# Performance work log

Hardware: AMD Instinct MI355X
Metric: run time of the kernel (lower is better)

Reference implementation:

```python
import jax, jax.numpy as jnp
import numpy as np

B, S, DIM, H = 2, 2048, 1024, 16
HD = DIM // H  # head dim = 64


def setup_inputs() -> dict:
    key = jax.random.key(0)
    ks = jax.random.split(key, 10)
    scale = 1.0 / np.sqrt(DIM)
    x = jax.random.normal(ks[0], (B, S, DIM), dtype=jnp.float32)
    # per-head projection weights stacked over heads: [H, DIM, HD]
    Wq = jax.random.normal(ks[1], (H, DIM, HD), dtype=jnp.float32) * scale
    bq = jax.random.normal(ks[2], (H, HD), dtype=jnp.float32) * 0.01
    Wk = jax.random.normal(ks[3], (H, DIM, HD), dtype=jnp.float32) * scale
    bk = jax.random.normal(ks[4], (H, HD), dtype=jnp.float32) * 0.01
    Wv = jax.random.normal(ks[5], (H, DIM, HD), dtype=jnp.float32) * scale
    bv = jax.random.normal(ks[6], (H, HD), dtype=jnp.float32) * 0.01
    # output linear: [DIM, DIM]
    Wo = jax.random.normal(ks[7], (DIM, DIM), dtype=jnp.float32) * scale
    bo = jax.random.normal(ks[8], (DIM,), dtype=jnp.float32) * 0.01
    return {"x": x, "Wq": Wq, "bq": bq, "Wk": Wk, "bk": bk,
            "Wv": Wv, "bv": bv, "Wo": Wo, "bo": bo}


def reference(x, Wq, bq, Wk, bk, Wv, bv, Wo, bo):
    # per-head projections: [B, H, S, HD]
    q = jnp.einsum('bsd,hde->bhse', x, Wq) + bq[None, :, None, :]
    k = jnp.einsum('bsd,hde->bhse', x, Wk) + bk[None, :, None, :]
    v = jnp.einsum('bsd,hde->bhse', x, Wv) + bv[None, :, None, :]
    # causal attention scores: [B, H, S, S], scaled by sqrt(head_dim)
    scores = jnp.einsum('bhse,bhte->bhst', q, k) / jnp.sqrt(jnp.float32(HD))
    causal = jnp.tril(jnp.ones((S, S), dtype=bool))
    scores = jnp.where(causal[None, None], scores, -jnp.inf)
    attn = jax.nn.softmax(scores, axis=-1)
    out = jnp.einsum('bhst,bhte->bhse', attn, v)  # [B, H, S, HD]
    # concat heads in order -> [B, S, DIM]
    out = out.transpose(0, 2, 1, 3).reshape(B, S, DIM)
    return out @ Wo + bo
```

## Files before the change

### kernel.cpp

```cpp
#include <hip/hip_runtime.h>

typedef _Float16 half8 __attribute__((ext_vector_type(8)));
typedef _Float16 half4 __attribute__((ext_vector_type(4)));
typedef float f32x4 __attribute__((ext_vector_type(4)));

#define MFMA32(a, b, c) __builtin_amdgcn_mfma_f32_16x16x32_f16((a), (b), (c), 0, 0, 0)
#define MFMA16(a, b, c) __builtin_amdgcn_mfma_f32_16x16x16f16((a), (b), (c), 0, 0, 0)

static constexpr int Bc = 2, Sc = 2048, DIMc = 1024, Hc = 16, HDc = 64;
static constexpr int Mc = Bc * Sc;
static constexpr int NQKV = 3 * DIMc;

__device__ __forceinline__ void gl_lds16(const _Float16* g, _Float16* l) {
  __builtin_amdgcn_global_load_lds(
      (const __attribute__((address_space(1))) void*)g,
      (__attribute__((address_space(3))) void*)l, 16, 0, 0);
}


__global__ __launch_bounds__(256) void k_prep_all(
    const float* __restrict__ x, const float* __restrict__ Wq,
    const float* __restrict__ Wk, const float* __restrict__ Wv,
    const float* __restrict__ Wo, _Float16* __restrict__ xh,
    _Float16* __restrict__ WallT, _Float16* __restrict__ WoT) {
  __shared__ float Ls[64 * 65];
  const int bx = blockIdx.x, tid = threadIdx.x;
  if (bx < 2048) {
    const int i = bx * 256 + tid;
    const float4* xf = (const float4*)x;
    float4 a = xf[i * 2], b = xf[i * 2 + 1];
    half8 hv;
    hv[0] = (_Float16)a.x; hv[1] = (_Float16)a.y;
    hv[2] = (_Float16)a.z; hv[3] = (_Float16)a.w;
    hv[4] = (_Float16)b.x; hv[5] = (_Float16)b.y;
    hv[6] = (_Float16)b.z; hv[7] = (_Float16)b.w;
    *(half8*)&xh[(size_t)i * 8] = hv;
    return;
  }
  int b2 = bx - 2048;
  if (b2 < 768) {
    const int dt = b2 & 15, ph = b2 >> 4;
    const int p = ph >> 4, h = ph & 15;
    const float* W = (p == 0) ? Wq : (p == 1) ? Wk : Wv;
    for (int c = tid; c < 4096; c += 256) {
      int dr = c >> 6, e = c & 63;
      Ls[e * 65 + dr] = W[h * 65536 + (dt * 64 + dr) * 64 + e];
    }
    __syncthreads();
    for (int c = tid; c < 4096; c += 256) {
      int e = c >> 6, dr = c & 63;
      WallT[(size_t)(p * 1024 + h * 64 + e) * 1024 + dt * 64 + dr] = (_Float16)Ls[e * 65 + dr];
    }
  } else {
    int b3 = b2 - 768;
    const int dt = b3 & 15, nt = b3 >> 4;
    for (int c = tid; c < 4096; c += 256) {
      int dr = c >> 6, nl = c & 63;
      Ls[nl * 65 + dr] = Wo[(dt * 64 + dr) * 1024 + nt * 64 + nl];
    }
    __syncthreads();
    for (int c = tid; c < 4096; c += 256) {
      int nl = c >> 6, dr = c & 63;
      WoT[(size_t)(nt * 64 + nl) * 1024 + dt * 64 + dr] = (_Float16)Ls[nl * 65 + dr];
    }
  }
}


#define STAGE_AB(buf, kk0)                                                     \
    for (int it = 0; it < 2; ++it) {                                           \
      int idx = it * 256 + tid;                                                \
      int row = idx >> 2, scb = (idx & 3) ^ ((row >> 1) & 3);                  \
      gl_lds16(&A[(size_t)(m0 + row) * DIMc + (kk0) + scb * 8],                \
               &As[buf][(it * 256 + wave * 64) * 8]);                          \
    }                                                                          \
    for (int it = 0; it < 2; ++it) {                                           \
      int idx = it * 256 + tid;                                                \
      int row = idx >> 2, scb = (idx & 3) ^ ((row >> 1) & 3);                  \
      gl_lds16(&Bt[(size_t)(n0 + row) * DIMc + (kk0) + scb * 8],               \
               &Bs[buf][(it * 256 + wave * 64) * 8]);                          \
    }

#define GEMM_CORE_COOP()                                                       \
  __shared__ _Float16 As[2][128 * 32];                                         \
  __shared__ _Float16 Bs[2][128 * 32];                                         \
  const int tid = threadIdx.x;                                                 \
  const int lane = tid & 63, wave = tid >> 6;                                  \
  const int quad = lane >> 4, mr = lane & 15;                                  \
  const int sl = quad ^ ((mr >> 1) & 3);                                       \
  const int wm = wave >> 1, wn = wave & 1;                                     \
  f32x4 acc[4][4];                                                             \
  for (int i = 0; i < 4; i++)                                                  \
    for (int j = 0; j < 4; j++) acc[i][j] = f32x4{0.f, 0.f, 0.f, 0.f};         \
  STAGE_AB(0, 0)                                                               \
  for (int k0 = 0; k0 < DIMc; k0 += 32) {                                      \
    const int cur = (k0 >> 5) & 1;                                             \
    if (k0 + 32 < DIMc) {                                                      \
      STAGE_AB(cur ^ 1, k0 + 32)                                               \
      asm volatile("s_waitcnt vmcnt(4)" ::: "memory");                         \
    } else {                                                                   \
      asm volatile("s_waitcnt vmcnt(0)" ::: "memory");                         \
    }                                                                          \
    __builtin_amdgcn_s_barrier();                                              \
    __builtin_amdgcn_sched_barrier(0);                                         \
    half8 af[4], bf[4];                                                        \
    for (int i = 0; i < 4; i++)                                                \
      af[i] = *(const half8*)&As[cur][(wm * 64 + i * 16 + mr) * 32 + sl * 8];  \
    for (int i = 0; i < 4; i++)                                                \
      bf[i] = *(const half8*)&Bs[cur][(wn * 64 + i * 16 + mr) * 32 + sl * 8];  \
    for (int i = 0; i < 4; i++)                                                \
      for (int j = 0; j < 4; j++) acc[i][j] = MFMA32(af[i], bf[j], acc[i][j]); \
    asm volatile("s_waitcnt lgkmcnt(0)" ::: "memory");                         \
    __builtin_amdgcn_s_barrier();                                              \
    __builtin_amdgcn_sched_barrier(0);                                         \
  }


#define STAGE_WP(buf, kk0)                                                     \
  {                                                                            \
    const int r_ = lane >> 2;                                                  \
    const int c_ = ((lane & 3) ^ ((r_ >> 1) & 3)) * 8;                         \
    for (int it = 0; it < 4; ++it)                                             \
      gl_lds16(&Arow[(size_t)(it * 16 + r_) * DIMc + (kk0) + c_],              \
               &SH[wave][buf][0][it * 512]);                                   \
    for (int it = 0; it < 4; ++it)                                             \
      gl_lds16(&Brow[(size_t)(it * 16 + r_) * DIMc + (kk0) + c_],              \
               &SH[wave][buf][1][it * 512]);                                   \
  }

#define COMPUTE_WP(buf)                                                        \
  {                                                                            \
    half8 af[4], bf[4];                                                        \
    for (int i = 0; i < 4; i++)                                                \
      af[i] = *(const half8*)&SH[wave][buf][0][(i * 16 + mr) * 32 + sl];       \
    for (int i = 0; i < 4; i++)                                                \
      bf[i] = *(const half8*)&SH[wave][buf][1][(i * 16 + mr) * 32 + sl];       \
    for (int i = 0; i < 4; i++)                                                \
      for (int j = 0; j < 4; j++) acc[i][j] = MFMA32(af[i], bf[j], acc[i][j]); \
  }

#define GEMM_CORE_WP()                                                         \
  __shared__ _Float16 SH[4][2][2][64 * 32];        \
  const int tid = threadIdx.x;                                                 \
  const int lane = tid & 63, wave = tid >> 6;                                  \
  const int quad = lane >> 4, mr = lane & 15;                                  \
  const int sl = (quad ^ ((mr >> 1) & 3)) * 8;                                 \
  const int wm = wave >> 1, wn = wave & 1;                                     \
  const _Float16* Arow = A + (size_t)(m0 + wm * 64) * DIMc;                    \
  const _Float16* Brow = Bt + (size_t)(n0 + wn * 64) * DIMc;                   \
  f32x4 acc[4][4];                                                             \
  for (int i = 0; i < 4; i++)                                                  \
    for (int j = 0; j < 4; j++) acc[i][j] = f32x4{0.f, 0.f, 0.f, 0.f};         \
  STAGE_WP(0, 0)                                                               \
  for (int k0 = 0; k0 < DIMc; k0 += 64) {                                      \
    STAGE_WP(1, k0 + 32)                                                       \
    asm volatile("s_waitcnt vmcnt(8)" ::: "memory");                           \
    __builtin_amdgcn_sched_barrier(0);                                         \
    COMPUTE_WP(0)                                                              \
    __builtin_amdgcn_sched_barrier(0);                                         \
    if (k0 + 64 < DIMc) {                                                      \
      STAGE_WP(0, k0 + 64)                                                     \
      asm volatile("s_waitcnt vmcnt(8)" ::: "memory");                         \
    } else {                                                                   \
      asm volatile("s_waitcnt vmcnt(0)" ::: "memory");                         \
    }                                                                          \
    __builtin_amdgcn_sched_barrier(0);                                         \
    COMPUTE_WP(1)                                                              \
    __builtin_amdgcn_sched_barrier(0);                                         \
  }

__global__ __launch_bounds__(256, 3) void k_gemm_qkv(
    const _Float16* __restrict__ xh, const _Float16* __restrict__ WallT,
    const float* __restrict__ bq, const float* __restrict__ bk,
    const float* __restrict__ bv, _Float16* __restrict__ qh,
    _Float16* __restrict__ kh, _Float16* __restrict__ vT) {
  const int bid = blockIdx.x;
  const int id = (bid & 7) * 96 + (bid >> 3);
  const bool qkrole = id < 512;
  const _Float16* A;
  const _Float16* Bt;
  int m0, n0;
  if (qkrole) {
    A = xh; Bt = WallT;
    n0 = (id & 15) * 128; m0 = (id >> 4) * 128;
  } else {
    int j = id - 512;
    A = WallT + (size_t)2048 * DIMc; Bt = xh;
    n0 = (j & 31) * 128; m0 = (j >> 5) * 128;
  }
  GEMM_CORE_COOP()
  if (qkrole) {
    for (int i = 0; i < 4; i++) {
      for (int j = 0; j < 4; j++) {
        int col = n0 + wn * 64 + j * 16 + mr;
        int p = col >> 10, rem = col & 1023;
        const float* bias = p ? bk : bq;
        _Float16* dst = p ? kh : qh;
        float bb = bias[rem];
        int h = rem >> 6, e = rem & 63;
        for (int r = 0; r < 4; r++) {
          int row = m0 + wm * 64 + i * 16 + quad * 4 + r;
          int b = row >> 11, s = row & 2047;
          dst[(((size_t)(b * Hc + h)) * Sc + s) * HDc + e] = (_Float16)(acc[i][j][r] + bb);
        }
      }
    }
  } else {
    for (int i = 0; i < 4; i++) {
      int rowb = m0 + wm * 64 + i * 16 + quad * 4;
      for (int j = 0; j < 4; j++) {
        int col = n0 + wn * 64 + j * 16 + mr;
        int b = col >> 11, s = col & 2047;
        for (int r = 0; r < 4; r++) {
          int row = rowb + r;
          vT[(size_t)(b * 1024 + row) * Sc + s] = (_Float16)(acc[i][j][r] + bv[row]);
        }
      }
    }
  }
}

__global__ __launch_bounds__(256, 2) void k_gemm_out(
    const _Float16* __restrict__ A, const _Float16* __restrict__ Bt,
    const float* __restrict__ bo, float* __restrict__ out) {
  const int fid = blockIdx.y * 8 + blockIdx.x;
  const int id = (fid & 7) * 32 + (fid >> 3);
  const int m0 = (id >> 3) * 128, n0 = (id & 7) * 128;
  GEMM_CORE_WP()
  for (int i = 0; i < 4; i++) {
    for (int j = 0; j < 4; j++) {
      int col = n0 + wn * 64 + j * 16 + mr;
      float bb = bo[col];
      for (int r = 0; r < 4; r++) {
        int row = m0 + wm * 64 + i * 16 + quad * 4 + r;
        out[(size_t)row * DIMc + col] = acc[i][j][r] + bb;
      }
    }
  }
}


__global__ __launch_bounds__(256, 2) void k_attn(
    const _Float16* __restrict__ qg, const _Float16* __restrict__ kg,
    const _Float16* __restrict__ vTg, _Float16* __restrict__ att) {
  const int bid = blockIdx.x;
  const int qt = 31 - (bid >> 5);
  const int bh = bid & 31;
  const int b = bh >> 4, h = bh & 15;
  const int tid = threadIdx.x, w = tid >> 6, lane = tid & 63;
  const int quad = lane >> 4, mr = lane & 15, m7 = mr & 7, m3 = mr & 3;
  const size_t base = (size_t)bh * (Sc * HDc);
  const _Float16* Kg = kg + base;
  const _Float16* Vg = vTg + ((size_t)b * 1024 + h * 64) * Sc;

  __shared__ _Float16 KV[4][2][2][2048];
  __shared__ float Lsh[4][64];

  const int q0 = qt * 64;
  const int ntt = 2 * qt + 2;
  const int myn = (w < ntt) ? ((ntt - 1 - w) >> 2) + 1 : 0;

  const _Float16 qsc = (_Float16)(0.125f * 1.44269504f);
  half8 aq[4][2];
  for (int qf = 0; qf < 4; ++qf)
    for (int c = 0; c < 2; ++c) {
      half8 v = *(const half8*)&qg[base + (size_t)(q0 + qf * 16 + mr) * 64 + c * 32 + quad * 8];
      for (int j = 0; j < 8; ++j) v[j] = v[j] * qsc;
      aq[qf][c] = v;
    }

  f32x4 o[4][4];
  f32x4 ol[4];
  for (int nf = 0; nf < 4; ++nf)
    for (int qf = 0; qf < 4; ++qf) o[nf][qf] = f32x4{0.f, 0.f, 0.f, 0.f};
  for (int qf = 0; qf < 4; ++qf) ol[qf] = f32x4{0.f, 0.f, 0.f, 0.f};
  const half4 ones = {(_Float16)1.f, (_Float16)1.f, (_Float16)1.f, (_Float16)1.f};

#define STAGE32(dst, tt)                                                       \
  {                                                                            \
    const _Float16* ks = Kg + (size_t)(tt) * 2048;                             \
    const _Float16* vs = Vg + (tt) * 32;                                       \
    for (int it = 0; it < 4; ++it) {                                           \
      int idx = it * 64 + lane;                                                \
      int row = idx >> 3, scb = (idx & 7) ^ (row & 7);                         \
      gl_lds16(ks + (size_t)row * 64 + scb * 8, (dst) + it * 512);             \
    }                                                                          \
    for (int it = 0; it < 4; ++it) {                                           \
      int idx = it * 64 + lane;                                                \
      int row = idx >> 2, scb = (idx & 3) ^ (row & 3);                         \
      gl_lds16(vs + (size_t)row * Sc + scb * 8, (dst) + 2048 + it * 512);      \
    }                                                                          \
  }

  if (myn > 0) STAGE32(&KV[w][0][0][0], w)
  asm volatile("s_waitcnt vmcnt(0)" ::: "memory");

  for (int i = 0; i < myn; ++i) {
    const int t = w + 4 * i;
    const _Float16* Kc = &KV[w][i & 1][0][0];
    const _Float16* Vc = &KV[w][i & 1][1][0];
    if (i + 1 < myn) STAGE32(&KV[w][(i + 1) & 1][0][0], t + 4)

    __builtin_amdgcn_s_setprio(1);
    const int dg = (t - 2 * qt) * 32;
    half4 pf[4][2];
    for (int kf = 0; kf < 2; ++kf) {
      const int r0 = (kf * 16 + mr) * 64;
      half8 k0 = *(const half8*)&Kc[r0 + ((quad ^ m7) * 8)];
      half8 k1 = *(const half8*)&Kc[r0 + (((quad ^ 4) ^ m7) * 8)];
      for (int qf = 0; qf < 4; ++qf) {
        f32x4 z = {0.f, 0.f, 0.f, 0.f};
        z = MFMA32(k0, aq[qf][0], z);
        z = MFMA32(k1, aq[qf][1], z);
        half4 pp;
        const int kvr = dg + kf * 16 + quad * 4;
        for (int r = 0; r < 4; ++r) {
          float p = __builtin_amdgcn_exp2f(z[r]);
          if (kvr + r > qf * 16 + mr) p = 0.f;
          pp[r] = (_Float16)p;
        }
        pf[qf][kf] = pp;
      }
    }

    for (int nf = 0; nf < 4; ++nf) {
      const int rb = (nf * 16 + mr) * 32;
      for (int kc = 0; kc < 2; ++kc) {
        int ch = kc * 2 + (quad >> 1);
        half4 vv = *(const half4*)&Vc[rb + ((ch ^ m3) * 8) + (quad & 1) * 4];
        for (int qf = 0; qf < 4; ++qf)
          o[nf][qf] = MFMA16(vv, pf[qf][kc], o[nf][qf]);
      }
    }
    for (int kc = 0; kc < 2; ++kc)
      for (int qf = 0; qf < 4; ++qf) ol[qf] = MFMA16(ones, pf[qf][kc], ol[qf]);
    __builtin_amdgcn_s_setprio(0);

    asm volatile("s_waitcnt vmcnt(0)" ::: "memory");
  }

  float* Osh = (float*)&KV[0][0][0][0];
  for (int nf = 0; nf < 4; ++nf)
    for (int qf = 0; qf < 4; ++qf)
      for (int r = 0; r < 4; ++r)
        Osh[w * 4096 + (nf * 16 + quad * 4 + r) * 64 + qf * 16 + mr] = o[nf][qf][r];
  if (quad == 0)
    for (int qf = 0; qf < 4; ++qf) Lsh[w][qf * 16 + mr] = ol[qf][0];
  __syncthreads();

  const int q = tid & 63, e0 = (tid >> 6) * 16;
  const float linv = 1.0f / (Lsh[0][q] + Lsh[1][q] + Lsh[2][q] + Lsh[3][q]);
  half8 o0, o1;
  for (int e = 0; e < 8; ++e) {
    float s = Osh[(e0 + e) * 64 + q] + Osh[4096 + (e0 + e) * 64 + q] +
              Osh[8192 + (e0 + e) * 64 + q] + Osh[12288 + (e0 + e) * 64 + q];
    o0[e] = (_Float16)(s * linv);
  }
  for (int e = 8; e < 16; ++e) {
    float s = Osh[(e0 + e) * 64 + q] + Osh[4096 + (e0 + e) * 64 + q] +
              Osh[8192 + (e0 + e) * 64 + q] + Osh[12288 + (e0 + e) * 64 + q];
    o1[e - 8] = (_Float16)(s * linv);
  }
  const size_t orow = ((size_t)(b * Sc + q0 + q)) * DIMc + h * 64 + e0;
  *(half8*)&att[orow] = o0;
  *(half8*)&att[orow + 8] = o1;
#undef STAGE32
}


extern "C" void kernel_launch(void* const* d_in, const int* in_sizes, int n_in,
                              void* d_out, int out_size, void* d_ws, size_t ws_size,
                              hipStream_t stream) {
  const float* x  = (const float*)d_in[0];
  const float* Wq = (const float*)d_in[1];
  const float* bq = (const float*)d_in[2];
  const float* Wk = (const float*)d_in[3];
  const float* bk = (const float*)d_in[4];
  const float* Wv = (const float*)d_in[5];
  const float* bv = (const float*)d_in[6];
  const float* Wo = (const float*)d_in[7];
  const float* bo = (const float*)d_in[8];
  float* out = (float*)d_out;

  _Float16* p = (_Float16*)d_ws;
  _Float16* xh    = p; p += (size_t)Mc * DIMc;
  _Float16* WallT = p; p += (size_t)NQKV * DIMc;
  _Float16* WoT   = p; p += (size_t)DIMc * DIMc;
  _Float16* qh    = p; p += (size_t)Bc * Hc * Sc * HDc;
  _Float16* kh    = p; p += (size_t)Bc * Hc * Sc * HDc;
  _Float16* vT    = p; p += (size_t)Bc * Hc * Sc * HDc;
  _Float16* atth  = p;

  k_prep_all<<<2048 + 768 + 256, 256, 0, stream>>>(x, Wq, Wk, Wv, Wo, xh, WallT, WoT);
  k_gemm_qkv<<<768, 256, 0, stream>>>(xh, WallT, bq, bk, bv, qh, kh, vT);
  k_attn<<<1024, 256, 0, stream>>>(qh, kh, vT, atth);
  k_gemm_out<<<dim3(DIMc / 128, Mc / 128), 256, 0, stream>>>(atth, WoT, bo, out);
}
```

Before: 181.3 us.

## Single-buffer K tiles and chunk epilogue reduction to raise attention occupancy

```diff
diff --git a/kernel.cpp b/kernel.cpp
--- a/kernel.cpp
+++ b/kernel.cpp
@@ -240,7 +240,7 @@
 }
 
 
-__global__ __launch_bounds__(256, 2) void k_attn(
+__global__ __launch_bounds__(256, 3) void k_attn(
     const _Float16* __restrict__ qg, const _Float16* __restrict__ kg,
     const _Float16* __restrict__ vTg, _Float16* __restrict__ att) {
   const int bid = blockIdx.x;
@@ -253,7 +253,8 @@
   const _Float16* Kg = kg + base;
   const _Float16* Vg = vTg + ((size_t)b * 1024 + h * 64) * Sc;
 
-  __shared__ _Float16 KV[4][2][2][2048];
+  __shared__ _Float16 Ks[4][2048];
+  __shared__ _Float16 Vs[4][2][2048];
   __shared__ float Lsh[4][64];
 
   const int q0 = qt * 64;
@@ -276,42 +277,51 @@
   for (int qf = 0; qf < 4; ++qf) ol[qf] = f32x4{0.f, 0.f, 0.f, 0.f};
   const half4 ones = {(_Float16)1.f, (_Float16)1.f, (_Float16)1.f, (_Float16)1.f};
 
-#define STAGE32(dst, tt)                                                       \
+#define STAGE_K(tt)                                                            \
   {                                                                            \
     const _Float16* ks = Kg + (size_t)(tt) * 2048;                             \
+    for (int it = 0; it < 4; ++it) {                                           \
+      int idx = it * 64 + lane;                                                \
+      int row = idx >> 3, scb = (idx & 7) ^ (row & 7);                         \
+      gl_lds16(ks + (size_t)row * 64 + scb * 8, &Ks[w][it * 512]);             \
+    }                                                                          \
+  }
+#define STAGE_V(dst, tt)                                                       \
+  {                                                                            \
     const _Float16* vs = Vg + (tt) * 32;                                       \
     for (int it = 0; it < 4; ++it) {                                           \
       int idx = it * 64 + lane;                                                \
-      int row = idx >> 3, scb = (idx & 7) ^ (row & 7);                         \
-      gl_lds16(ks + (size_t)row * 64 + scb * 8, (dst) + it * 512);             \
+      int row = idx >> 2, scb = (idx & 3) ^ (row & 3);                         \
+      gl_lds16(vs + (size_t)row * Sc + scb * 8, (dst) + it * 512);             \
     }                                                                          \
-    for (int it = 0; it < 4; ++it) {                                           \
-      int idx = it * 64 + lane;                                                \
-      int row = idx >> 2, scb = (idx & 3) ^ (row & 3);                         \
-      gl_lds16(vs + (size_t)row * Sc + scb * 8, (dst) + 2048 + it * 512);      \
-    }                                                                          \
-  }
-
-  if (myn > 0) STAGE32(&KV[w][0][0][0], w)
+  }
+
+  if (myn > 0) { STAGE_K(w) STAGE_V(&Vs[w][0][0], w) }
   asm volatile("s_waitcnt vmcnt(0)" ::: "memory");
 
   for (int i = 0; i < myn; ++i) {
     const int t = w + 4 * i;
-    const _Float16* Kc = &KV[w][i & 1][0][0];
-    const _Float16* Vc = &KV[w][i & 1][1][0];
-    if (i + 1 < myn) STAGE32(&KV[w][(i + 1) & 1][0][0], t + 4)
+    const _Float16* Vc = &Vs[w][i & 1][0];
+    if (i + 1 < myn) STAGE_V(&Vs[w][(i + 1) & 1][0], t + 4)
+
+    half8 kA[2][2];
+    for (int kf = 0; kf < 2; ++kf) {
+      const int r0 = (kf * 16 + mr) * 64;
+      kA[kf][0] = *(const half8*)&Ks[w][r0 + ((quad ^ m7) * 8)];
+      kA[kf][1] = *(const half8*)&Ks[w][r0 + (((quad ^ 4) ^ m7) * 8)];
+    }
+    asm volatile("s_waitcnt lgkmcnt(0)" ::: "memory");
+    __builtin_amdgcn_sched_barrier(0);
+    if (i + 1 < myn) STAGE_K(t + 4)
 
     __builtin_amdgcn_s_setprio(1);
     const int dg = (t - 2 * qt) * 32;
     half4 pf[4][2];
     for (int kf = 0; kf < 2; ++kf) {
-      const int r0 = (kf * 16 + mr) * 64;
-      half8 k0 = *(const half8*)&Kc[r0 + ((quad ^ m7) * 8)];
-      half8 k1 = *(const half8*)&Kc[r0 + (((quad ^ 4) ^ m7) * 8)];
       for (int qf = 0; qf < 4; ++qf) {
         f32x4 z = {0.f, 0.f, 0.f, 0.f};
-        z = MFMA32(k0, aq[qf][0], z);
-        z = MFMA32(k1, aq[qf][1], z);
+        z = MFMA32(kA[kf][0], aq[qf][0], z);
+        z = MFMA32(kA[kf][1], aq[qf][1], z);
         half4 pp;
         const int kvr = dg + kf * 16 + quad * 4;
         for (int r = 0; r < 4; ++r) {
@@ -339,32 +349,31 @@
     asm volatile("s_waitcnt vmcnt(0)" ::: "memory");
   }
 
-  float* Osh = (float*)&KV[0][0][0][0];
-  for (int nf = 0; nf < 4; ++nf)
-    for (int qf = 0; qf < 4; ++qf)
-      for (int r = 0; r < 4; ++r)
-        Osh[w * 4096 + (nf * 16 + quad * 4 + r) * 64 + qf * 16 + mr] = o[nf][qf][r];
   if (quad == 0)
     for (int qf = 0; qf < 4; ++qf) Lsh[w][qf * 16 + mr] = ol[qf][0];
   __syncthreads();
 
-  const int q = tid & 63, e0 = (tid >> 6) * 16;
+  const int q = tid & 63, eg = tid >> 6;
   const float linv = 1.0f / (Lsh[0][q] + Lsh[1][q] + Lsh[2][q] + Lsh[3][q]);
-  half8 o0, o1;
-  for (int e = 0; e < 8; ++e) {
-    float s = Osh[(e0 + e) * 64 + q] + Osh[4096 + (e0 + e) * 64 + q] +
-              Osh[8192 + (e0 + e) * 64 + q] + Osh[12288 + (e0 + e) * 64 + q];
-    o0[e] = (_Float16)(s * linv);
-  }
-  for (int e = 8; e < 16; ++e) {
-    float s = Osh[(e0 + e) * 64 + q] + Osh[4096 + (e0 + e) * 64 + q] +
-              Osh[8192 + (e0 + e) * 64 + q] + Osh[12288 + (e0 + e) * 64 + q];
-    o1[e - 8] = (_Float16)(s * linv);
-  }
-  const size_t orow = ((size_t)(b * Sc + q0 + q)) * DIMc + h * 64 + e0;
-  *(half8*)&att[orow] = o0;
-  *(half8*)&att[orow + 8] = o1;
-#undef STAGE32
+  float* Osh = (float*)&Ks[0][0];
+  const size_t orow = ((size_t)(b * Sc + q0 + q)) * DIMc + h * 64;
+  for (int nf = 0; nf < 4; ++nf) {
+    for (int qf = 0; qf < 4; ++qf)
+      for (int r = 0; r < 4; ++r)
+        Osh[(w * 16 + quad * 4 + r) * 64 + qf * 16 + mr] = o[nf][qf][r];
+    __syncthreads();
+    half4 ov;
+    for (int r = 0; r < 4; ++r) {
+      int e = eg * 4 + r;
+      float s = Osh[e * 64 + q] + Osh[(16 + e) * 64 + q] +
+                Osh[(32 + e) * 64 + q] + Osh[(48 + e) * 64 + q];
+      ov[r] = (_Float16)(s * linv);
+    }
+    *(half4*)&att[orow + nf * 16 + eg * 4] = ov;
+    __syncthreads();
+  }
+#undef STAGE_K
+#undef STAGE_V
 }
 
 
```

New measurement: 179.8 us, median of 2. No clear change (-0.8%).
